# Optimization experiments

Hardware: AMD Instinct MI355X
Metric: run time of the kernel (lower is better)

Reference implementation:

```python
import jax, jax.numpy as jnp
import numpy as np

B, IN_DIM, K, OUT_DIM = 512, 16384, 32, 16
DIMS = [8192, 4096, 2048]  # floor(dim/factor) per layer, factor=2


def setup_inputs() -> dict:
    key = jax.random.key(0)
    ks = jax.random.split(key, 16)
    inp = {"x": jax.random.normal(ks[0], (B, IN_DIM), dtype=jnp.float32)}
    prev = IN_DIM
    std = (2.0 / K) ** 0.5
    for i, d in enumerate(DIMS):
        inp[f"w{i}"] = jax.random.normal(ks[1 + i], (d, K), dtype=jnp.float32) * std
        inp[f"b{i}"] = jnp.zeros((1, d), dtype=jnp.float32)
        inp[f"knn{i}"] = jax.random.randint(ks[8 + i], (d, K), 0, prev, dtype=jnp.int64)
        prev = d
    inp["fc_w"] = jax.random.normal(ks[12], (DIMS[-1], OUT_DIM), dtype=jnp.float32) * (1.0 / DIMS[-1] ** 0.5)
    inp["fc_b"] = jnp.zeros((OUT_DIM,), dtype=jnp.float32)
    return inp


def reference(x, w0, b0, w1, b1, w2, b2, fc_w, fc_b, knn0, knn1, knn2):
    # Each layer: gather K neighbors per output unit, weighted sum over K, bias, ReLU.
    for w, b, knn in ((w0, b0, knn0), (w1, b1, knn1), (w2, b2, knn2)):
        g = x[:, knn]                              # (B, dim_i, K) irregular gather
        x = jax.nn.relu(jnp.einsum('bdk,dk->bd', g, w) + b)
    return x @ fc_w + fc_b                         # fc_angle
```

## Files before the change

### kernel.cpp

```cpp
#include <hip/hip_runtime.h>
#include <hip/hip_fp16.h>

#define BATCH   512
#define IN_DIM  16384
#define KNN     32
#define NCHUNK  8
#define CHUNK   64

typedef __attribute__((ext_vector_type(4))) _Float16 half4v;

__global__ __launch_bounds__(256) void transpose_h(const float* __restrict__ in,
                                                   _Float16* __restrict__ out) {
    __shared__ float tile[32][33];
    const int bx = blockIdx.x * 32;
    const int by = blockIdx.y * 32;
    const int tx = threadIdx.x & 31;
    const int ty = threadIdx.x >> 5;
#pragma unroll
    for (int j = 0; j < 32; j += 8)
        tile[ty + j][tx] = in[(size_t)(by + ty + j) * IN_DIM + bx + tx];
    __syncthreads();
    const int r = threadIdx.x >> 3;
    const int c = (threadIdx.x & 7) * 4;
    half4v h;
    h[0] = (_Float16)tile[c + 0][r];
    h[1] = (_Float16)tile[c + 1][r];
    h[2] = (_Float16)tile[c + 2][r];
    h[3] = (_Float16)tile[c + 3][r];
    *(half4v*)(out + (size_t)(bx + r) * BATCH + by + c) = h;
}

__global__ __launch_bounds__(64) void lcn_layer_h(const _Float16* __restrict__ xt,
                                                  const float* __restrict__ w,
                                                  const float* __restrict__ bias,
                                                  const int* __restrict__ knn,
                                                  _Float16* __restrict__ yt) {
    const int d  = blockIdx.x >> 3;
    const int b  = (blockIdx.x & 7) * CHUNK + threadIdx.x;
    const int*   kp = knn + d * KNN;
    const float* wp = w   + d * KNN;
    float acc = 0.f;
#pragma unroll
    for (int k = 0; k < KNN; ++k) {
        const int   idx = kp[k];
        const float wv  = wp[k];
        acc += wv * (float)xt[(size_t)idx * BATCH + b];
    }
    acc = fmaxf(acc + bias[d], 0.f);
    yt[(size_t)d * BATCH + b] = (_Float16)acc;
}

__global__ __launch_bounds__(256) void fc_partial(const _Float16* __restrict__ y2t,
                                                  const float* __restrict__ fcw,
                                                  float* __restrict__ part) {
    const int o  = blockIdx.x & 15;
    const int bh = (blockIdx.x >> 4) & 1;
    const int ch = blockIdx.x >> 5;
    const int b  = bh * 256 + threadIdx.x;
    const int d0 = ch * 256;
    float a0 = 0.f, a1 = 0.f, a2 = 0.f, a3 = 0.f;
#pragma unroll 4
    for (int d = d0; d < d0 + 256; d += 4) {
        a0 += (float)y2t[(size_t)(d + 0) * BATCH + b] * fcw[(d + 0) * 16 + o];
        a1 += (float)y2t[(size_t)(d + 1) * BATCH + b] * fcw[(d + 1) * 16 + o];
        a2 += (float)y2t[(size_t)(d + 2) * BATCH + b] * fcw[(d + 2) * 16 + o];
        a3 += (float)y2t[(size_t)(d + 3) * BATCH + b] * fcw[(d + 3) * 16 + o];
    }
    part[((size_t)b * 16 + o) * 8 + ch] = (a0 + a1) + (a2 + a3);
}

__global__ __launch_bounds__(256) void fc_final(const float* __restrict__ part,
                                                const float* __restrict__ fcb,
                                                float* __restrict__ out) {
    const int t = blockIdx.x * 256 + threadIdx.x;
    const float4 p0 = *(const float4*)(part + (size_t)t * 8);
    const float4 p1 = *(const float4*)(part + (size_t)t * 8 + 4);
    out[t] = ((p0.x + p0.y) + (p0.z + p0.w)) + ((p1.x + p1.y) + (p1.z + p1.w))
             + fcb[t & 15];
}

extern "C" void kernel_launch(void* const* d_in, const int* in_sizes, int n_in,
                              void* d_out, int out_size, void* d_ws, size_t ws_size,
                              hipStream_t stream) {
    const float* x    = (const float*)d_in[0];
    const float* w0   = (const float*)d_in[1];
    const float* b0   = (const float*)d_in[2];
    const int*   knn0 = (const int*)  d_in[3];
    const float* w1   = (const float*)d_in[4];
    const float* b1   = (const float*)d_in[5];
    const int*   knn1 = (const int*)  d_in[6];
    const float* w2   = (const float*)d_in[7];
    const float* b2   = (const float*)d_in[8];
    const int*   knn2 = (const int*)  d_in[9];
    const float* fcw  = (const float*)d_in[10];
    const float* fcb  = (const float*)d_in[11];
    float* out = (float*)d_out;

    char* ws = (char*)d_ws;
    _Float16* xt   = (_Float16*)(ws);
    _Float16* y0t  = (_Float16*)(ws + ((size_t)16 << 20));
    _Float16* y1t  = (_Float16*)(ws + ((size_t)24 << 20));
    _Float16* y2t  = (_Float16*)(ws + ((size_t)28 << 20));
    float*    part = (float*)   (ws + ((size_t)30 << 20));

    transpose_h<<<dim3(IN_DIM / 32, BATCH / 32), 256, 0, stream>>>(x, xt);
    lcn_layer_h<<<8192 * NCHUNK, 64, 0, stream>>>(xt,  w0, b0, knn0, y0t);
    lcn_layer_h<<<4096 * NCHUNK, 64, 0, stream>>>(y0t, w1, b1, knn1, y1t);
    lcn_layer_h<<<2048 * NCHUNK, 64, 0, stream>>>(y1t, w2, b2, knn2, y2t);
    fc_partial<<<256, 256, 0, stream>>>(y2t, fcw, part);
    fc_final<<<32, 256, 0, stream>>>(part, fcb, out);
}
```

Baseline: 70.32 us.

## Compute multiple output units per thread and vectorize batch pairs in LCN layers

New measurement: 82.74 us. +17.7%, slower.

```diff
diff --git a/kernel.cpp b/kernel.cpp
--- a/kernel.cpp
+++ b/kernel.cpp
@@ -4,10 +4,9 @@
 #define BATCH   512
 #define IN_DIM  16384
 #define KNN     32
-#define NCHUNK  8
-#define CHUNK   64
 
 typedef __attribute__((ext_vector_type(4))) _Float16 half4v;
+typedef __attribute__((ext_vector_type(2))) _Float16 half2v;
 
 __global__ __launch_bounds__(256) void transpose_h(const float* __restrict__ in,
                                                    _Float16* __restrict__ out) {
@@ -30,24 +29,70 @@
     *(half4v*)(out + (size_t)(bx + r) * BATCH + by + c) = h;
 }
 
-__global__ __launch_bounds__(64) void lcn_layer_h(const _Float16* __restrict__ xt,
-                                                  const float* __restrict__ w,
-                                                  const float* __restrict__ bias,
-                                                  const int* __restrict__ knn,
-                                                  _Float16* __restrict__ yt) {
-    const int d  = blockIdx.x >> 3;
-    const int b  = (blockIdx.x & 7) * CHUNK + threadIdx.x;
-    const int*   kp = knn + d * KNN;
-    const float* wp = w   + d * KNN;
-    float acc = 0.f;
+template<int DPER>
+__global__ __launch_bounds__(64) void lcn_h1(const _Float16* __restrict__ xt,
+                                             const float* __restrict__ w,
+                                             const float* __restrict__ bias,
+                                             const int* __restrict__ knn,
+                                             _Float16* __restrict__ yt) {
+    const int dg = blockIdx.x >> 3;
+    const int b  = (blockIdx.x & 7) * 64 + threadIdx.x;
+    const _Float16* xb = xt + b;
+    const int*   kp = knn + (size_t)dg * DPER * KNN;
+    const float* wp = w   + (size_t)dg * DPER * KNN;
+    float acc[DPER];
 #pragma unroll
+    for (int j = 0; j < DPER; ++j) acc[j] = 0.f;
+#pragma unroll 4
     for (int k = 0; k < KNN; ++k) {
-        const int   idx = kp[k];
-        const float wv  = wp[k];
-        acc += wv * (float)xt[(size_t)idx * BATCH + b];
+#pragma unroll
+        for (int j = 0; j < DPER; ++j) {
+            const int   idx = kp[j * KNN + k];
+            const float wv  = wp[j * KNN + k];
+            acc[j] += wv * (float)xb[(size_t)idx * BATCH];
+        }
     }
-    acc = fmaxf(acc + bias[d], 0.f);
-    yt[(size_t)d * BATCH + b] = (_Float16)acc;
+#pragma unroll
+    for (int j = 0; j < DPER; ++j) {
+        const int d = dg * DPER + j;
+        yt[(size_t)d * BATCH + b] = (_Float16)fmaxf(acc[j] + bias[d], 0.f);
+    }
+}
+
+template<int DPER>
+__global__ __launch_bounds__(64) void lcn_h2(const _Float16* __restrict__ xt,
+                                             const float* __restrict__ w,
+                                             const float* __restrict__ bias,
+                                             const int* __restrict__ knn,
+                                             _Float16* __restrict__ yt) {
+    const int dg = blockIdx.x >> 2;
+    const int b  = (blockIdx.x & 3) * 128 + 2 * threadIdx.x;
+    const _Float16* xb = xt + b;
+    const int*   kp = knn + (size_t)dg * DPER * KNN;
+    const float* wp = w   + (size_t)dg * DPER * KNN;
+    float ax[DPER], ay[DPER];
+#pragma unroll
+    for (int j = 0; j < DPER; ++j) { ax[j] = 0.f; ay[j] = 0.f; }
+#pragma unroll 4
+    for (int k = 0; k < KNN; ++k) {
+#pragma unroll
+        for (int j = 0; j < DPER; ++j) {
+            const int   idx = kp[j * KNN + k];
+            const float wv  = wp[j * KNN + k];
+            const half2v v  = *(const half2v*)(xb + (size_t)idx * BATCH);
+            ax[j] += wv * (float)v[0];
+            ay[j] += wv * (float)v[1];
+        }
+    }
+#pragma unroll
+    for (int j = 0; j < DPER; ++j) {
+        const int d = dg * DPER + j;
+        const float bv = bias[d];
+        half2v r;
+        r[0] = (_Float16)fmaxf(ax[j] + bv, 0.f);
+        r[1] = (_Float16)fmaxf(ay[j] + bv, 0.f);
+        *(half2v*)(yt + (size_t)d * BATCH + b) = r;
+    }
 }
 
 __global__ __launch_bounds__(256) void fc_partial(const _Float16* __restrict__ y2t,
@@ -104,9 +149,9 @@
     float*    part = (float*)   (ws + ((size_t)30 << 20));
 
     transpose_h<<<dim3(IN_DIM / 32, BATCH / 32), 256, 0, stream>>>(x, xt);
-    lcn_layer_h<<<8192 * NCHUNK, 64, 0, stream>>>(xt,  w0, b0, knn0, y0t);
-    lcn_layer_h<<<4096 * NCHUNK, 64, 0, stream>>>(y0t, w1, b1, knn1, y1t);
-    lcn_layer_h<<<2048 * NCHUNK, 64, 0, stream>>>(y1t, w2, b2, knn2, y2t);
+    lcn_h1<8><<<(8192 / 8) * 8, 64, 0, stream>>>(xt,  w0, b0, knn0, y0t);
+    lcn_h2<4><<<(4096 / 4) * 4, 64, 0, stream>>>(y0t, w1, b1, knn1, y1t);
+    lcn_h2<4><<<(2048 / 4) * 4, 64, 0, stream>>>(y1t, w2, b2, knn2, y2t);
     fc_partial<<<256, 256, 0, stream>>>(y2t, fcw, part);
     fc_final<<<32, 256, 0, stream>>>(part, fcb, out);
 }
```
